# Kernel optimization log

Hardware: AMD Instinct MI355X
Metric: run time of the kernel (lower is better)

Reference implementation:

```python
import jax, jax.numpy as jnp
import numpy as np

N_NODES = 50000
N_EDGES = 800000
N_GRAPHS = 64
D_IN = 128
D_HID = 128
D_OUT = 32
N_LAYERS = 2


def setup_inputs() -> dict:
    key = jax.random.key(0)
    ks = jax.random.split(key, 12)
    x = jax.random.normal(ks[0], (N_NODES, D_IN), dtype=jnp.float32)
    edge_index = jax.random.randint(ks[1], (2, N_EDGES), 0, N_NODES, dtype=jnp.int64)
    batch = jnp.sort(jax.random.randint(ks[2], (N_NODES,), 0, N_GRAPHS, dtype=jnp.int64))
    s = 1.0 / np.sqrt(D_HID)
    return {
        "x": x,
        "edge_index": edge_index,
        "batch": batch,
        "conv_w_rel": jax.random.normal(ks[3], (N_LAYERS, D_IN, D_HID), dtype=jnp.float32) * s,
        "conv_b_rel": jax.random.normal(ks[4], (N_LAYERS, D_HID), dtype=jnp.float32) * s,
        "conv_w_root": jax.random.normal(ks[5], (N_LAYERS, D_IN, D_HID), dtype=jnp.float32) * s,
        "sage_w_l": jax.random.normal(ks[6], (N_LAYERS, D_HID, D_HID), dtype=jnp.float32) * s,
        "sage_b_l": jax.random.normal(ks[7], (N_LAYERS, D_HID), dtype=jnp.float32) * s,
        "sage_w_r": jax.random.normal(ks[8], (N_LAYERS, D_HID, D_HID), dtype=jnp.float32) * s,
        "fc_w": jax.random.normal(ks[9], (D_HID, D_OUT), dtype=jnp.float32) * s,
        "fc_b": jax.random.normal(ks[10], (D_OUT,), dtype=jnp.float32) * s,
    }


def reference(x, edge_index, batch, conv_w_rel, conv_b_rel, conv_w_root,
              sage_w_l, sage_b_l, sage_w_r, fc_w, fc_b):
    N = x.shape[0]
    src, dst = edge_index[0], edge_index[1]
    # StandardScaler: per-feature standardization (population std)
    mu = jnp.mean(x, axis=0)
    sd = jnp.std(x, axis=0)
    h = (x - mu) / sd
    # Stacked GraphConv layers: lin_rel(sum-aggr neighbors) + lin_root(x), then ReLU
    for l in range(conv_w_rel.shape[0]):
        agg = jax.ops.segment_sum(h[src], dst, num_segments=N)  # [N, D]
        h = jax.nn.relu(agg @ conv_w_rel[l] + conv_b_rel[l] + h @ conv_w_root[l])
    # GraphSAGE: SAGEConv layers (mean aggregation), ReLU between layers only
    deg = jax.ops.segment_sum(jnp.ones((src.shape[0],), dtype=h.dtype), dst, num_segments=N)
    deg = jnp.clip(deg, 1.0)[:, None]  # [N, 1]
    L = sage_w_l.shape[0]
    for l in range(L):
        agg = jax.ops.segment_sum(h[src], dst, num_segments=N) / deg  # mean over neighbors
        h_new = agg @ sage_w_l[l] + sage_b_l[l] + h @ sage_w_r[l]
        h = jax.nn.relu(h_new) if l < L - 1 else h_new
    # global_mean_pool over graphs
    sums = jax.ops.segment_sum(h, batch, num_segments=N_GRAPHS)  # [G, D]
    cnt = jax.ops.segment_sum(jnp.ones((N,), dtype=h.dtype), batch, num_segments=N_GRAPHS)
    pooled = sums / jnp.clip(cnt, 1.0)[:, None]
    return pooled @ fc_w + fc_b  # [G, D_OUT]
```

## Files before the change

### kernel.cpp

```cpp
#include <hip/hip_runtime.h>

#define N_NODES 50000
#define N_EDGES 800000
#define N_GRAPHS 64
#define DH 128
#define DOUT 32

typedef __attribute__((ext_vector_type(8))) short bf16x8;
typedef __attribute__((ext_vector_type(4))) float f32x4;

__device__ __forceinline__ unsigned short f2bf(float f) {
    union { float f; unsigned int u; } x;
    x.f = f;
    unsigned int u = x.u;
    u += 0x7FFFu + ((u >> 16) & 1u);
    return (unsigned short)(u >> 16);
}

__device__ __forceinline__ float bf2f(unsigned short s) {
    union { unsigned int u; float f; } x;
    x.u = ((unsigned int)s) << 16;
    return x.f;
}

#define STAT_BLKS 512
__global__ __launch_bounds__(256) void stats_kernel(const float* __restrict__ x,
                                                    float* __restrict__ partial) {
    __shared__ float4 shs[256];
    __shared__ float4 shq[256];
    const int tid = threadIdx.x;
    const int rowgrp = tid >> 5;
    const int cq = tid & 31;
    float4 s = make_float4(0.f, 0.f, 0.f, 0.f);
    float4 q = make_float4(0.f, 0.f, 0.f, 0.f);
#pragma unroll 4
    for (int r = blockIdx.x * 8 + rowgrp; r < N_NODES; r += STAT_BLKS * 8) {
        const float4 v = *reinterpret_cast<const float4*>(x + (size_t)r * DH + cq * 4);
        s.x += v.x; s.y += v.y; s.z += v.z; s.w += v.w;
        q.x = fmaf(v.x, v.x, q.x); q.y = fmaf(v.y, v.y, q.y);
        q.z = fmaf(v.z, v.z, q.z); q.w = fmaf(v.w, v.w, q.w);
    }
    shs[tid] = s; shq[tid] = q;
    __syncthreads();
    for (int off = 128; off >= 32; off >>= 1) {
        if (tid < off) {
            float4 a = shs[tid], b = shs[tid + off];
            a.x += b.x; a.y += b.y; a.z += b.z; a.w += b.w;
            shs[tid] = a;
            float4 c = shq[tid], d = shq[tid + off];
            c.x += d.x; c.y += d.y; c.z += d.z; c.w += d.w;
            shq[tid] = c;
        }
        __syncthreads();
    }
    if (tid < 32) {
        const float4 a = shs[tid];
        const float4 c = shq[tid];
        const float sv[4] = {a.x, a.y, a.z, a.w};
        const float qv[4] = {c.x, c.y, c.z, c.w};
#pragma unroll
        for (int j = 0; j < 4; ++j) {
            const int col = tid * 4 + j;
            partial[(size_t)col * STAT_BLKS + blockIdx.x] = sv[j];
            partial[(size_t)(128 + col) * STAT_BLKS + blockIdx.x] = qv[j];
        }
    }
}

__global__ __launch_bounds__(128) void finalize_stats_kernel(const float* __restrict__ partial,
                                                             float* __restrict__ stat) {
    const int c = threadIdx.x;
    const float4* ps = reinterpret_cast<const float4*>(partial + (size_t)c * STAT_BLKS);
    const float4* pq = reinterpret_cast<const float4*>(partial + (size_t)(128 + c) * STAT_BLKS);
    float s = 0.f, q = 0.f;
#pragma unroll 8
    for (int b = 0; b < STAT_BLKS / 4; ++b) {
        const float4 v = ps[b];
        s += v.x + v.y + v.z + v.w;
        const float4 w = pq[b];
        q += w.x + w.y + w.z + w.w;
    }
    const float inv_n = 1.0f / (float)N_NODES;
    const float mu = s * inv_n;
    const float var = q * inv_n - mu * mu;
    const float sd = sqrtf(fmaxf(var, 1e-20f));
    stat[256 + c] = mu;
    stat[384 + c] = 1.0f / sd;
}

__global__ void standardize_kernel(const float* __restrict__ x,
                                   const float* __restrict__ stat,
                                   unsigned short* __restrict__ h) {
    const size_t i = (size_t)blockIdx.x * blockDim.x + threadIdx.x;
    const int c4 = (int)(i & 31) << 2;
    const float4 v = reinterpret_cast<const float4*>(x)[i];
    const float4 m = *reinterpret_cast<const float4*>(stat + 256 + c4);
    const float4 is = *reinterpret_cast<const float4*>(stat + 384 + c4);
    ushort4 o;
    o.x = f2bf((v.x - m.x) * is.x);
    o.y = f2bf((v.y - m.y) * is.y);
    o.z = f2bf((v.z - m.z) * is.z);
    o.w = f2bf((v.w - m.w) * is.w);
    reinterpret_cast<ushort4*>(h)[i] = o;
}

__global__ void count_deg_kernel(const int* __restrict__ dst, int* __restrict__ deg_i) {
    int e = blockIdx.x * blockDim.x + threadIdx.x;
    if (e < N_EDGES) atomicAdd(&deg_i[dst[e]], 1);
}

#define SCAN_BLK 256
#define SCAN_NBLK ((N_NODES + SCAN_BLK - 1) / SCAN_BLK)

__global__ __launch_bounds__(SCAN_BLK) void scan_local_kernel(const int* __restrict__ deg_i,
                                                              int* __restrict__ row_ptr,
                                                              int* __restrict__ bsum) {
    __shared__ int sh[SCAN_BLK];
    const int tid = threadIdx.x;
    const int idx = blockIdx.x * SCAN_BLK + tid;
    const int v = (idx < N_NODES) ? deg_i[idx] : 0;
    sh[tid] = v;
    __syncthreads();
#pragma unroll
    for (int off = 1; off < SCAN_BLK; off <<= 1) {
        const int t = (tid >= off) ? sh[tid - off] : 0;
        __syncthreads();
        sh[tid] += t;
        __syncthreads();
    }
    if (idx < N_NODES) row_ptr[idx] = sh[tid] - v;
    if (tid == SCAN_BLK - 1) bsum[blockIdx.x] = sh[tid];
}

__global__ __launch_bounds__(SCAN_BLK) void scan_bsum_kernel(int* __restrict__ bsum) {
    __shared__ int sh[SCAN_BLK];
    const int tid = threadIdx.x;
    const int v = (tid < SCAN_NBLK) ? bsum[tid] : 0;
    sh[tid] = v;
    __syncthreads();
#pragma unroll
    for (int off = 1; off < SCAN_BLK; off <<= 1) {
        const int t = (tid >= off) ? sh[tid - off] : 0;
        __syncthreads();
        sh[tid] += t;
        __syncthreads();
    }
    if (tid < SCAN_NBLK) bsum[tid] = sh[tid] - v;
}

__global__ __launch_bounds__(SCAN_BLK) void scan_finalize_kernel(const int* __restrict__ deg_i,
                                                                 const int* __restrict__ bsum,
                                                                 int* __restrict__ row_ptr,
                                                                 int* __restrict__ cursor,
                                                                 float* __restrict__ deg_inv) {
    const int tid = threadIdx.x;
    const int idx = blockIdx.x * SCAN_BLK + tid;
    if (idx < N_NODES) {
        const int excl = row_ptr[idx] + bsum[blockIdx.x];
        row_ptr[idx] = excl;
        cursor[idx] = excl;
        const int d = deg_i[idx];
        deg_inv[idx] = 1.0f / (float)(d > 1 ? d : 1);
    }
    if (idx == 0) row_ptr[N_NODES] = N_EDGES;
}

__global__ void scatter_kernel(const int* __restrict__ src, const int* __restrict__ dst,
                               int* __restrict__ cursor, int* __restrict__ csr_src) {
    int e = blockIdx.x * blockDim.x + threadIdx.x;
    if (e < N_EDGES) {
        const int pos = atomicAdd(&cursor[dst[e]], 1);
        csr_src[pos] = src[e];
    }
}

__global__ __launch_bounds__(256) void aggregate_csr_kernel(const unsigned short* __restrict__ h,
                                                            const int* __restrict__ row_ptr,
                                                            const int* __restrict__ csr_src,
                                                            const float* __restrict__ deg_inv,
                                                            unsigned short* __restrict__ agg,
                                                            const int useScale) {
    const int node = blockIdx.x * 4 + (threadIdx.x >> 6);
    if (node >= N_NODES) return;
    const int lane = threadIdx.x & 63;
    const int beg = row_ptr[node];
    const int end = row_ptr[node + 1];
    float a0 = 0.f, a1 = 0.f;
    float b0 = 0.f, b1 = 0.f;
    for (int chunk = beg; chunk < end; chunk += 64) {
        const int cnt = min(64, end - chunk);
        const int sv = (lane < cnt) ? csr_src[chunk + lane] : 0;
        int j = 0;
        for (; j + 4 <= cnt; j += 4) {
            const int s0 = __shfl(sv, j + 0);
            const int s1 = __shfl(sv, j + 1);
            const int s2 = __shfl(sv, j + 2);
            const int s3 = __shfl(sv, j + 3);
            const unsigned int v0 = *reinterpret_cast<const unsigned int*>(h + (size_t)s0 * DH + lane * 2);
            const unsigned int v1 = *reinterpret_cast<const unsigned int*>(h + (size_t)s1 * DH + lane * 2);
            const unsigned int v2 = *reinterpret_cast<const unsigned int*>(h + (size_t)s2 * DH + lane * 2);
            const unsigned int v3 = *reinterpret_cast<const unsigned int*>(h + (size_t)s3 * DH + lane * 2);
            union { unsigned int u; float f; } t;
            t.u = v0 << 16; a0 += t.f;  t.u = v0 & 0xFFFF0000u; a1 += t.f;
            t.u = v1 << 16; b0 += t.f;  t.u = v1 & 0xFFFF0000u; b1 += t.f;
            t.u = v2 << 16; a0 += t.f;  t.u = v2 & 0xFFFF0000u; a1 += t.f;
            t.u = v3 << 16; b0 += t.f;  t.u = v3 & 0xFFFF0000u; b1 += t.f;
        }
        for (; j < cnt; ++j) {
            const int s = __shfl(sv, j);
            const unsigned int v = *reinterpret_cast<const unsigned int*>(h + (size_t)s * DH + lane * 2);
            union { unsigned int u; float f; } t;
            t.u = v << 16; a0 += t.f;  t.u = v & 0xFFFF0000u; a1 += t.f;
        }
    }
    float o0 = a0 + b0, o1 = a1 + b1;
    if (useScale) {
        const float sc = deg_inv[node];
        o0 *= sc; o1 *= sc;
    }
    const unsigned int packed = (unsigned int)f2bf(o0) | ((unsigned int)f2bf(o1) << 16);
    reinterpret_cast<unsigned int*>(agg + (size_t)node * DH)[lane] = packed;
}

__global__ void pack_w_kernel(const float* __restrict__ cwr, const float* __restrict__ cwroot,
                              const float* __restrict__ swl, const float* __restrict__ swr,
                              unsigned short* __restrict__ wfrag) {
    const int g = blockIdx.x * blockDim.x + threadIdx.x;
    if (g >= 16384) return;
    const int lane = g & 63;
    const int n = (g >> 6) & 7;
    const int t = (g >> 9) & 3;
    const int phase = (g >> 11) & 1;
    const int layer = (g >> 12) & 3;
    const float* W1 = (layer < 2) ? (cwr + layer * 16384) : (swl + (layer - 2) * 16384);
    const float* W2 = (layer < 2) ? (cwroot + layer * 16384) : (swr + (layer - 2) * 16384);
    const float* W = phase ? W2 : W1;
    const int col = n * 16 + (lane & 15);
    const int k0 = t * 32 + (lane >> 4) * 8;
    unsigned short v[8];
#pragma unroll
    for (int j = 0; j < 8; ++j) v[j] = f2bf(W[(size_t)(k0 + j) * DH + col]);
    unsigned short* dst = wfrag + ((((size_t)g)) * 8);
#pragma unroll
    for (int j = 0; j < 8; ++j) dst[j] = v[j];
}

__global__ __launch_bounds__(256) void fused_layer_mfma_kernel(
    const unsigned short* __restrict__ A1, const unsigned short* __restrict__ A2,
    const unsigned short* __restrict__ Wf, const float* __restrict__ bias,
    unsigned short* __restrict__ Cb, float* __restrict__ Cf, const int relu) {
    const int wid = threadIdx.x >> 6;
    const int lane = threadIdx.x & 63;
    const int row0 = blockIdx.x * 64 + wid * 16;
    const int arow = row0 + (lane & 15);
    const int koff = (lane >> 4) * 8;
    const bool rowOK = (arow < N_NODES);

    f32x4 acc[8];
#pragma unroll
    for (int n = 0; n < 8; ++n) acc[n] = (f32x4){0.f, 0.f, 0.f, 0.f};

#pragma unroll
    for (int phase = 0; phase < 2; ++phase) {
        const unsigned short* Ar = (phase ? A2 : A1) + (size_t)arow * DH;
        const unsigned short* Wp = Wf + (size_t)phase * (4 * 8 * 64 * 8);
#pragma unroll
        for (int t = 0; t < 4; ++t) {
            bf16x8 af = {};
            if (rowOK) af = *reinterpret_cast<const bf16x8*>(Ar + t * 32 + koff);
            const unsigned short* wt = Wp + (((size_t)t * 8) * 64 + lane) * 8;
#pragma unroll
            for (int n = 0; n < 8; ++n) {
                const bf16x8 bfv = *reinterpret_cast<const bf16x8*>(wt + (size_t)n * 64 * 8);
                acc[n] = __builtin_amdgcn_mfma_f32_16x16x32_bf16(af, bfv, acc[n], 0, 0, 0);
            }
        }
    }

    const int crow0 = row0 + (lane >> 4) * 4;
    const int ccol = lane & 15;
#pragma unroll
    for (int n = 0; n < 8; ++n) {
        const int col = n * 16 + ccol;
        const float bv = bias[col];
#pragma unroll
        for (int r = 0; r < 4; ++r) {
            const int grow = crow0 + r;
            if (grow >= N_NODES) continue;
            float v = acc[n][r] + bv;
            if (relu) {
                v = fmaxf(v, 0.f);
                Cb[(size_t)grow * DH + col] = f2bf(v);
            } else {
                Cf[(size_t)grow * DH + col] = v;
            }
        }
    }
}

#define POOL_BLOCKS 512
__global__ __launch_bounds__(128) void pool_seg_kernel(const float* __restrict__ h,
                                                       const int* __restrict__ batch,
                                                       float* __restrict__ pooled,
                                                       float* __restrict__ cnt) {
    const int c = threadIdx.x;
    const int nper = (N_NODES + POOL_BLOCKS - 1) / POOL_BLOCKS;
    const int n0 = blockIdx.x * nper;
    const int n1 = min(n0 + nper, N_NODES);
    if (n0 >= n1) return;
    float acc = 0.f;
    int g = batch[n0];
    int runlen = 0;
    for (int n = n0; n < n1; ++n) {
        const int bg = batch[n];
        if (bg != g) {
            atomicAdd(&pooled[(size_t)g * DH + c], acc);
            if (c == 0) atomicAdd(&cnt[g], (float)runlen);
            acc = 0.f; runlen = 0; g = bg;
        }
        acc += h[(size_t)n * DH + c];
        ++runlen;
    }
    atomicAdd(&pooled[(size_t)g * DH + c], acc);
    if (c == 0) atomicAdd(&cnt[g], (float)runlen);
}

__global__ void final_kernel(const float* __restrict__ pooled, const float* __restrict__ cnt,
                             const float* __restrict__ fcw, const float* __restrict__ fcb,
                             float* __restrict__ out) {
    const int g = blockIdx.x;
    const int j = threadIdx.x;
    if (j >= DOUT) return;
    const float inv = 1.0f / fmaxf(cnt[g], 1.0f);
    float acc = fcb[j];
    for (int d = 0; d < DH; ++d)
        acc = fmaf(pooled[(size_t)g * DH + d] * inv, fcw[(size_t)d * DOUT + j], acc);
    out[(size_t)g * DOUT + j] = acc;
}

extern "C" void kernel_launch(void* const* d_in, const int* in_sizes, int n_in,
                              void* d_out, int out_size, void* d_ws, size_t ws_size,
                              hipStream_t stream) {
    const float* x = (const float*)d_in[0];
    const int* ei = (const int*)d_in[1];
    const int* batch = (const int*)d_in[2];
    const float* conv_w_rel = (const float*)d_in[3];
    const float* conv_b_rel = (const float*)d_in[4];
    const float* conv_w_root = (const float*)d_in[5];
    const float* sage_w_l = (const float*)d_in[6];
    const float* sage_b_l = (const float*)d_in[7];
    const float* sage_w_r = (const float*)d_in[8];
    const float* fc_w = (const float*)d_in[9];
    const float* fc_b = (const float*)d_in[10];
    float* out = (float*)d_out;

    const int* src = ei;
    const int* dst = ei + N_EDGES;

    const size_t NHB = (size_t)N_NODES * DH * sizeof(unsigned short);
    const size_t NFB = (size_t)N_NODES * DH * sizeof(float);
    char* p = (char*)d_ws;
    unsigned short* hb0 = (unsigned short*)p; p += NHB;
    unsigned short* hb1 = (unsigned short*)p; p += NHB;
    unsigned short* aggb = (unsigned short*)p; p += NHB;
    float* hF = (float*)p; p += NFB;
    float* deg_inv = (float*)p; p += ((size_t)N_NODES * sizeof(float) + 255) & ~(size_t)255;
    float* stat = (float*)p; p += 512 * sizeof(float);
    float* pooled = (float*)p; p += (size_t)N_GRAPHS * DH * sizeof(float);
    float* cnt = (float*)p; p += ((size_t)N_GRAPHS * sizeof(float) + 255) & ~(size_t)255;
    int* deg_i = (int*)p; p += ((size_t)N_NODES * sizeof(int) + 255) & ~(size_t)255;
    int* row_ptr = (int*)p; p += ((size_t)(N_NODES + 1) * sizeof(int) + 255) & ~(size_t)255;
    int* cursor = (int*)p; p += ((size_t)N_NODES * sizeof(int) + 255) & ~(size_t)255;
    int* bsum = (int*)p; p += ((size_t)SCAN_BLK * sizeof(int) + 255) & ~(size_t)255;
    float* partial = (float*)p; p += (size_t)256 * STAT_BLKS * sizeof(float);
    unsigned short* wfrag = (unsigned short*)p; p += (size_t)4 * 32768 * sizeof(unsigned short);
    int* csr_src = (int*)p; p += (size_t)N_EDGES * sizeof(int);

    hipLaunchKernelGGL(stats_kernel, dim3(STAT_BLKS), dim3(256), 0, stream, x, partial);
    hipLaunchKernelGGL(finalize_stats_kernel, dim3(1), dim3(DH), 0, stream, partial, stat);
    hipLaunchKernelGGL(standardize_kernel, dim3((N_NODES * DH / 4) / 256), dim3(256), 0, stream,
                       x, stat, hb0);

    hipLaunchKernelGGL(pack_w_kernel, dim3(64), dim3(256), 0, stream,
                       conv_w_rel, conv_w_root, sage_w_l, sage_w_r, wfrag);

    hipMemsetAsync(deg_i, 0, (size_t)N_NODES * sizeof(int), stream);
    hipLaunchKernelGGL(count_deg_kernel, dim3((N_EDGES + 255) / 256), dim3(256), 0, stream,
                       dst, deg_i);
    hipLaunchKernelGGL(scan_local_kernel, dim3(SCAN_NBLK), dim3(SCAN_BLK), 0, stream,
                       deg_i, row_ptr, bsum);
    hipLaunchKernelGGL(scan_bsum_kernel, dim3(1), dim3(SCAN_BLK), 0, stream, bsum);
    hipLaunchKernelGGL(scan_finalize_kernel, dim3(SCAN_NBLK), dim3(SCAN_BLK), 0, stream,
                       deg_i, bsum, row_ptr, cursor, deg_inv);
    hipLaunchKernelGGL(scatter_kernel, dim3((N_EDGES + 255) / 256), dim3(256), 0, stream,
                       src, dst, cursor, csr_src);

    const float* Bs[4] = {conv_b_rel, conv_b_rel + 128, sage_b_l, sage_b_l + 128};

    unsigned short* curb = hb0;
    unsigned short* nxtb = hb1;
    const dim3 aggGrid((N_NODES + 3) / 4);
    const dim3 gemmGrid((N_NODES + 63) / 64);
    for (int l = 0; l < 4; ++l) {
        hipLaunchKernelGGL(aggregate_csr_kernel, aggGrid, dim3(256), 0, stream,
                           curb, row_ptr, csr_src, deg_inv, aggb, (l >= 2) ? 1 : 0);
        hipLaunchKernelGGL(fused_layer_mfma_kernel, gemmGrid, dim3(256), 0, stream,
                           aggb, curb, wfrag + (size_t)l * 32768, Bs[l],
                           (l < 3) ? nxtb : (unsigned short*)nullptr,
                           (l < 3) ? (float*)nullptr : hF,
                           (l < 3) ? 1 : 0);
        unsigned short* t = curb; curb = nxtb; nxtb = t;
    }

    hipMemsetAsync(pooled, 0, ((size_t)N_GRAPHS * DH + N_GRAPHS) * sizeof(float), stream);
    hipLaunchKernelGGL(pool_seg_kernel, dim3(POOL_BLOCKS), dim3(DH), 0, stream,
                       hF, batch, pooled, cnt);
    hipLaunchKernelGGL(final_kernel, dim3(N_GRAPHS), dim3(64), 0, stream,
                       pooled, cnt, fc_w, fc_b, out);
}
```

Baseline: 367.4 us.

## Partition CSR scatter by destination range per XCD and widen gather unroll

The edge scatter now runs as a grid-stride kernel in which each block handles only the edges whose destinations fall in one of eight node ranges, with the range picked from blockIdx modulo 8. The aim is that atomics and csr writes for a given range stay in one XCD's L2. The price is that every range group reads the whole dst array, so dst is read eight times. Separately, the aggregation gather loop is unrolled to eight loads in flight with a single accumulator pair, and some unused helpers and names are cleaned up.

```diff
diff --git a/kernel.cpp b/kernel.cpp
--- a/kernel.cpp
+++ b/kernel.cpp
@@ -15,12 +15,6 @@
     unsigned int u = x.u;
     u += 0x7FFFu + ((u >> 16) & 1u);
     return (unsigned short)(u >> 16);
-}
-
-__device__ __forceinline__ float bf2f(unsigned short s) {
-    union { unsigned int u; float f; } x;
-    x.u = ((unsigned int)s) << 16;
-    return x.f;
 }
 
 #define STAT_BLKS 512
@@ -165,12 +159,24 @@
     if (idx == 0) row_ptr[N_NODES] = N_EDGES;
 }
 
-__global__ void scatter_kernel(const int* __restrict__ src, const int* __restrict__ dst,
-                               int* __restrict__ cursor, int* __restrict__ csr_src) {
-    int e = blockIdx.x * blockDim.x + threadIdx.x;
-    if (e < N_EDGES) {
-        const int pos = atomicAdd(&cursor[dst[e]], 1);
-        csr_src[pos] = src[e];
+#define NXCD 8
+#define RANGE_NODES ((N_NODES + NXCD - 1) / NXCD)
+#define SC_SLICES 104
+__global__ __launch_bounds__(256) void scatter_ranged_kernel(const int* __restrict__ src,
+                                                             const int* __restrict__ dst,
+                                                             int* __restrict__ cursor,
+                                                             int* __restrict__ csr_src) {
+    const int range = blockIdx.x & (NXCD - 1);
+    const int slice = blockIdx.x >> 3;
+    const int lo = range * RANGE_NODES;
+    const int hi = min(lo + RANGE_NODES, N_NODES);
+    const int stride = SC_SLICES * 256;
+    for (int e = slice * 256 + threadIdx.x; e < N_EDGES; e += stride) {
+        const int d = dst[e];
+        if (d >= lo && d < hi) {
+            const int pos = atomicAdd(&cursor[d], 1);
+            csr_src[pos] = src[e];
+        }
     }
 }
 
@@ -186,34 +192,34 @@
     const int beg = row_ptr[node];
     const int end = row_ptr[node + 1];
     float a0 = 0.f, a1 = 0.f;
-    float b0 = 0.f, b1 = 0.f;
     for (int chunk = beg; chunk < end; chunk += 64) {
         const int cnt = min(64, end - chunk);
         const int sv = (lane < cnt) ? csr_src[chunk + lane] : 0;
         int j = 0;
-        for (; j + 4 <= cnt; j += 4) {
-            const int s0 = __shfl(sv, j + 0);
-            const int s1 = __shfl(sv, j + 1);
-            const int s2 = __shfl(sv, j + 2);
-            const int s3 = __shfl(sv, j + 3);
-            const unsigned int v0 = *reinterpret_cast<const unsigned int*>(h + (size_t)s0 * DH + lane * 2);
-            const unsigned int v1 = *reinterpret_cast<const unsigned int*>(h + (size_t)s1 * DH + lane * 2);
-            const unsigned int v2 = *reinterpret_cast<const unsigned int*>(h + (size_t)s2 * DH + lane * 2);
-            const unsigned int v3 = *reinterpret_cast<const unsigned int*>(h + (size_t)s3 * DH + lane * 2);
-            union { unsigned int u; float f; } t;
-            t.u = v0 << 16; a0 += t.f;  t.u = v0 & 0xFFFF0000u; a1 += t.f;
-            t.u = v1 << 16; b0 += t.f;  t.u = v1 & 0xFFFF0000u; b1 += t.f;
-            t.u = v2 << 16; a0 += t.f;  t.u = v2 & 0xFFFF0000u; a1 += t.f;
-            t.u = v3 << 16; b0 += t.f;  t.u = v3 & 0xFFFF0000u; b1 += t.f;
+        for (; j + 8 <= cnt; j += 8) {
+            int ss[8];
+#pragma unroll
+            for (int u = 0; u < 8; ++u) ss[u] = __shfl(sv, j + u);
+            unsigned int vv[8];
+#pragma unroll
+            for (int u = 0; u < 8; ++u)
+                vv[u] = *reinterpret_cast<const unsigned int*>(h + (size_t)ss[u] * DH + lane * 2);
+#pragma unroll
+            for (int u = 0; u < 8; ++u) {
+                union { unsigned int x; float f; } t;
+                t.x = vv[u] << 16; a0 += t.f;
+                t.x = vv[u] & 0xFFFF0000u; a1 += t.f;
+            }
         }
         for (; j < cnt; ++j) {
             const int s = __shfl(sv, j);
             const unsigned int v = *reinterpret_cast<const unsigned int*>(h + (size_t)s * DH + lane * 2);
-            union { unsigned int u; float f; } t;
-            t.u = v << 16; a0 += t.f;  t.u = v & 0xFFFF0000u; a1 += t.f;
-        }
-    }
-    float o0 = a0 + b0, o1 = a1 + b1;
+            union { unsigned int x; float f; } t;
+            t.x = v << 16; a0 += t.f;
+            t.x = v & 0xFFFF0000u; a1 += t.f;
+        }
+    }
+    float o0 = a0, o1 = a1;
     if (useScale) {
         const float sc = deg_inv[node];
         o0 *= sc; o1 *= sc;
@@ -240,9 +246,9 @@
     unsigned short v[8];
 #pragma unroll
     for (int j = 0; j < 8; ++j) v[j] = f2bf(W[(size_t)(k0 + j) * DH + col]);
-    unsigned short* dst = wfrag + ((((size_t)g)) * 8);
-#pragma unroll
-    for (int j = 0; j < 8; ++j) dst[j] = v[j];
+    unsigned short* dstp = wfrag + ((size_t)g * 8);
+#pragma unroll
+    for (int j = 0; j < 8; ++j) dstp[j] = v[j];
 }
 
 __global__ __launch_bounds__(256) void fused_layer_mfma_kernel(
@@ -392,7 +398,7 @@
     hipLaunchKernelGGL(scan_bsum_kernel, dim3(1), dim3(SCAN_BLK), 0, stream, bsum);
     hipLaunchKernelGGL(scan_finalize_kernel, dim3(SCAN_NBLK), dim3(SCAN_BLK), 0, stream,
                        deg_i, bsum, row_ptr, cursor, deg_inv);
-    hipLaunchKernelGGL(scatter_kernel, dim3((N_EDGES + 255) / 256), dim3(256), 0, stream,
+    hipLaunchKernelGGL(scatter_ranged_kernel, dim3(NXCD * SC_SLICES), dim3(256), 0, stream,
                        src, dst, cursor, csr_src);
 
     const float* Bs[4] = {conv_b_rel, conv_b_rel + 128, sage_b_l, sage_b_l + 128};
```

Measured after the change: 358.4 us. -2.4%, faster.
